# Optimization experiments

Measured on AMD Instinct MI355X. Metric: run time of the kernel, lower is better.

The kernel has to match this reference:

```python
import jax, jax.numpy as jnp
import numpy as np

MASK_THR = 0.005   # cfg.mask_thr
SIGMA = 2.0        # cfg.sigma (gaussian kernel)
N, G, H, W = 500, 128, 200, 304


def setup_inputs() -> dict:
    key = jax.random.key(0)
    k1, k2, k3, k4, k5, k6 = jax.random.split(key, 6)
    return {
        "cate_scores": jax.random.uniform(k1, (N,), jnp.float32),
        "seg_preds_x": jax.random.uniform(k2, (G, H, W), jnp.float32),
        "seg_preds_y": jax.random.uniform(k3, (G, H, W), jnp.float32),
        "cate_labels": jax.random.randint(k4, (N,), 0, 80),
        "x_inds": jax.random.randint(k5, (N,), 0, G),
        "y_inds": jax.random.randint(k6, (N,), 0, G),
    }


def reference(cate_scores, seg_preds_x, seg_preds_y, cate_labels, x_inds, y_inds):
    # --- SOLO decoupled mask decoding: irregular grid-index gather ---
    mask_x = seg_preds_x[x_inds]                 # [N,H,W]
    mask_y = seg_preds_y[y_inds]                 # [N,H,W]
    soft = mask_x * mask_y                       # seg_masks_soft
    hard = (soft > MASK_THR).astype(soft.dtype)  # seg_masks (binary)
    sum_masks = hard.sum((1, 2))                 # [N] mask areas
    # mask-quality rescoring
    seg_score = (soft * hard).sum((1, 2)) / jnp.maximum(sum_masks, 1.0)
    scores = cate_scores * seg_score

    # --- Matrix NMS (gaussian kernel) ---
    flat = hard.reshape(N, -1)                   # [N, H*W]
    inter = flat @ flat.T                        # [N,N] intersection areas
    union = sum_masks[:, None] + sum_masks[None, :] - inter
    iou = jnp.triu(inter / jnp.maximum(union, 1e-6), k=1)
    label_eq = jnp.triu((cate_labels[:, None] == cate_labels[None, :]).astype(soft.dtype), k=1)
    decay_iou = iou * label_eq                   # same-class IoU, upper tri
    comp_iou = decay_iou.max(0)                  # [N] max IoU with higher-scored same-class mask
    decay_matrix = jnp.exp(-SIGMA * decay_iou ** 2)
    comp_matrix = jnp.exp(-SIGMA * comp_iou ** 2)[:, None]  # expand(n,n).T in torch
    decay_coef = (decay_matrix / comp_matrix).min(0)         # [N]
    return scores * decay_coef
```

## Files before the change

kernel.cpp:

```cpp
#include <hip/hip_runtime.h>


#define N_DET 500
#define HW    (200 * 304)
#define NGROUP 238
#define NWORDS 952
#define NW2    476
#define MASK_THR 0.005f
#define SIGMA 2.0f

__global__ __launch_bounds__(512) void maskgen_kernel(
    const float* __restrict__ seg_x, const float* __restrict__ seg_y,
    const int* __restrict__ x_inds, const int* __restrict__ y_inds,
    unsigned long long* __restrict__ packed,
    float* __restrict__ part_sum,
    int*   __restrict__ part_cnt)
{
    const int b = blockIdx.x;
    const int n = b >> 1;
    const int s = b & 1;
    const float* __restrict__ rx = seg_x + (size_t)x_inds[n] * HW;
    const float* __restrict__ ry = seg_y + (size_t)y_inds[n] * HW;
    unsigned long long* __restrict__ pk = packed + (size_t)n * NWORDS;

    const int tid  = threadIdx.x;
    const int lane = tid & 63;
    const int wav  = tid >> 6;

    float ssum = 0.0f;
    int   cnt  = 0;
    const int gend = s * 119 + 119;
    for (int g = s * 119 + wav; g < gend; g += 8) {
        const int base = (g << 8) + (lane << 2);
        float4 x, y;
        if (base + 3 < HW) {
            x = *(const float4*)(rx + base);
            y = *(const float4*)(ry + base);
        } else {
            x = make_float4(0.f, 0.f, 0.f, 0.f);
            y = x;
        }
        const float p0 = x.x * y.x, p1 = x.y * y.y, p2 = x.z * y.z, p3 = x.w * y.w;
        const bool h0 = p0 > MASK_THR, h1 = p1 > MASK_THR,
                   h2 = p2 > MASK_THR, h3 = p3 > MASK_THR;
        const unsigned long long m0 = __ballot(h0), m1 = __ballot(h1),
                                 m2 = __ballot(h2), m3 = __ballot(h3);
        if (lane < 4) {
            const unsigned long long mv = (lane == 0) ? m0 : (lane == 1) ? m1
                                        : (lane == 2) ? m2 : m3;
            pk[(g << 2) + lane] = mv;
        }
        ssum += (h0 ? p0 : 0.f) + (h1 ? p1 : 0.f) + (h2 ? p2 : 0.f) + (h3 ? p3 : 0.f);
        cnt  += (int)h0 + (int)h1 + (int)h2 + (int)h3;
    }
    #pragma unroll
    for (int off = 32; off; off >>= 1) {
        ssum += __shfl_down(ssum, off);
        cnt  += __shfl_down(cnt,  off);
    }
    __shared__ float s_s[8];
    __shared__ int   s_c[8];
    if (lane == 0) { s_s[wav] = ssum; s_c[wav] = cnt; }
    __syncthreads();
    if (tid == 0) {
        float S = 0.f; int C = 0;
        #pragma unroll
        for (int q = 0; q < 8; ++q) { S += s_s[q]; C += s_c[q]; }
        part_sum[b] = S;
        part_cnt[b] = C;
    }
}

__global__ __launch_bounds__(512) void finalize_kernel(
    const float* __restrict__ part_sum, const int* __restrict__ part_cnt,
    const float* __restrict__ cate_scores,
    float* __restrict__ sum_masks, float* __restrict__ scores)
{
    const int n = threadIdx.x;
    if (n < N_DET) {
        const float S = part_sum[2 * n] + part_sum[2 * n + 1];
        const int   C = part_cnt[2 * n] + part_cnt[2 * n + 1];
        const float sm = (float)C;
        sum_masks[n] = sm;
        scores[n] = cate_scores[n] * (S / fmaxf(sm, 1.0f));
    }
}

__global__ __launch_bounds__(256) void pair_iou_kernel(
    const unsigned long long* __restrict__ packed,
    const float* __restrict__ sum_masks,
    const int* __restrict__ labels,
    float* __restrict__ d2col,
    float* __restrict__ comp2)
{
    const int j   = blockIdx.x;
    const int tid = threadIdx.x;
    const int lane = tid & 63, wav = tid >> 6;

    __shared__ int   s_lab[N_DET];
    __shared__ float s_sm[N_DET];
    __shared__ int   s_list[N_DET];
    __shared__ int   s_cnt;
    __shared__ float s_max[4];

    if (tid == 0) s_cnt = 0;
    for (int i = tid; i < N_DET; i += 256) {
        s_lab[i] = labels[i];
        s_sm[i]  = sum_masks[i];
        d2col[(size_t)j * N_DET + i] = 0.0f;
    }
    __syncthreads();

    const int   lj = s_lab[j];
    const float sj = s_sm[j];
    for (int i = tid; i < j; i += 256)
        if (s_lab[i] == lj) { const int p = atomicAdd(&s_cnt, 1); s_list[p] = i; }
    __syncthreads();
    const int cnt = s_cnt;

    const ulonglong2* __restrict__ pj2 = (const ulonglong2*)(packed + (size_t)j * NWORDS);
    ulonglong2 bj[8];
    #pragma unroll
    for (int t = 0; t < 8; ++t) {
        const int w = lane + (t << 6);
        if (w < NW2) bj[t] = pj2[w];
        else { bj[t].x = 0ull; bj[t].y = 0ull; }
    }

    float wmax = 0.0f;
    for (int p = wav; p < cnt; p += 4) {
        const int i = s_list[p];
        const ulonglong2* __restrict__ pi2 = (const ulonglong2*)(packed + (size_t)i * NWORDS);
        int part = 0;
        #pragma unroll
        for (int t = 0; t < 8; ++t) {
            const int w = lane + (t << 6);
            if (w < NW2) {
                const ulonglong2 a = pi2[w];
                part += __popcll(a.x & bj[t].x) + __popcll(a.y & bj[t].y);
            }
        }
        #pragma unroll
        for (int off = 32; off; off >>= 1) part += __shfl_down(part, off);
        if (lane == 0) {
            const float uni = s_sm[i] + sj - (float)part;
            const float iou = (float)part / fmaxf(uni, 1e-6f);
            d2col[(size_t)j * N_DET + i] = iou * iou;
            wmax = fmaxf(wmax, iou);
        }
    }
    if (lane == 0) s_max[wav] = wmax;
    __syncthreads();
    if (tid == 0) {
        const float c = fmaxf(fmaxf(s_max[0], s_max[1]), fmaxf(s_max[2], s_max[3]));
        comp2[j] = c * c;
    }
}

__global__ __launch_bounds__(64) void decay_kernel(
    const float* __restrict__ d2col,
    const float* __restrict__ comp2,
    const float* __restrict__ scores,
    float* __restrict__ out)
{
    const int j = blockIdx.x;
    const int lane = threadIdx.x;
    float m = 1e30f;
    for (int i = lane; i < N_DET; i += 64)
        m = fminf(m, comp2[i] - d2col[(size_t)j * N_DET + i]);
    #pragma unroll
    for (int off = 32; off; off >>= 1)
        m = fminf(m, __shfl_down(m, off));
    if (lane == 0) out[j] = scores[j] * expf(SIGMA * m);
}

extern "C" void kernel_launch(void* const* d_in, const int* in_sizes, int n_in,
                              void* d_out, int out_size, void* d_ws, size_t ws_size,
                              hipStream_t stream) {
    const float* cate_scores = (const float*)d_in[0];
    const float* seg_x       = (const float*)d_in[1];
    const float* seg_y       = (const float*)d_in[2];
    const int*   labels      = (const int*)d_in[3];
    const int*   x_inds      = (const int*)d_in[4];
    const int*   y_inds      = (const int*)d_in[5];
    float* out = (float*)d_out;

    char* ws = (char*)d_ws;
    unsigned long long* packed = (unsigned long long*)(ws + 0);
    float* d2col     = (float*)(ws + 3808000);
    float* part_sum  = (float*)(ws + 4808000);
    int*   part_cnt  = (int*)  (ws + 4812000);
    float* scores    = (float*)(ws + 4816000);
    float* comp2     = (float*)(ws + 4818000);
    float* sum_masks = (float*)(ws + 4820000);

    maskgen_kernel <<<N_DET * 2, 512, 0, stream>>>(seg_x, seg_y, x_inds, y_inds,
                                                   packed, part_sum, part_cnt);
    finalize_kernel<<<1, 512, 0, stream>>>(part_sum, part_cnt, cate_scores,
                                           sum_masks, scores);
    pair_iou_kernel<<<N_DET, 256, 0, stream>>>(packed, sum_masks, labels, d2col, comp2);
    decay_kernel   <<<N_DET, 64, 0, stream>>>(d2col, comp2, scores, out);
}
```

Baseline: 131.3 us.

## Tile mask generation over pixels to share grid rows across all detections

```diff
diff --git a/kernel.cpp b/kernel.cpp
--- a/kernel.cpp
+++ b/kernel.cpp
@@ -3,9 +3,11 @@
 
 #define N_DET 500
 #define HW    (200 * 304)
-#define NGROUP 238
-#define NWORDS 952
-#define NW2    476
+#define TILE  64
+#define NT    (HW / TILE)
+#define NWORDS NT
+#define NW2   (NWORDS / 2)
+#define LSTR  65
 #define MASK_THR 0.005f
 #define SIGMA 2.0f
 
@@ -16,70 +18,65 @@
     float* __restrict__ part_sum,
     int*   __restrict__ part_cnt)
 {
-    const int b = blockIdx.x;
-    const int n = b >> 1;
-    const int s = b & 1;
-    const float* __restrict__ rx = seg_x + (size_t)x_inds[n] * HW;
-    const float* __restrict__ ry = seg_y + (size_t)y_inds[n] * HW;
-    unsigned long long* __restrict__ pk = packed + (size_t)n * NWORDS;
-
-    const int tid  = threadIdx.x;
-    const int lane = tid & 63;
-    const int wav  = tid >> 6;
-
-    float ssum = 0.0f;
-    int   cnt  = 0;
-    const int gend = s * 119 + 119;
-    for (int g = s * 119 + wav; g < gend; g += 8) {
-        const int base = (g << 8) + (lane << 2);
-        float4 x, y;
-        if (base + 3 < HW) {
-            x = *(const float4*)(rx + base);
-            y = *(const float4*)(ry + base);
-        } else {
-            x = make_float4(0.f, 0.f, 0.f, 0.f);
-            y = x;
-        }
-        const float p0 = x.x * y.x, p1 = x.y * y.y, p2 = x.z * y.z, p3 = x.w * y.w;
-        const bool h0 = p0 > MASK_THR, h1 = p1 > MASK_THR,
-                   h2 = p2 > MASK_THR, h3 = p3 > MASK_THR;
-        const unsigned long long m0 = __ballot(h0), m1 = __ballot(h1),
-                                 m2 = __ballot(h2), m3 = __ballot(h3);
-        if (lane < 4) {
-            const unsigned long long mv = (lane == 0) ? m0 : (lane == 1) ? m1
-                                        : (lane == 2) ? m2 : m3;
-            pk[(g << 2) + lane] = mv;
-        }
-        ssum += (h0 ? p0 : 0.f) + (h1 ? p1 : 0.f) + (h2 ? p2 : 0.f) + (h3 ? p3 : 0.f);
-        cnt  += (int)h0 + (int)h1 + (int)h2 + (int)h3;
-    }
-    #pragma unroll
-    for (int off = 32; off; off >>= 1) {
-        ssum += __shfl_down(ssum, off);
-        cnt  += __shfl_down(cnt,  off);
-    }
-    __shared__ float s_s[8];
-    __shared__ int   s_c[8];
-    if (lane == 0) { s_s[wav] = ssum; s_c[wav] = cnt; }
-    __syncthreads();
-    if (tid == 0) {
-        float S = 0.f; int C = 0;
-        #pragma unroll
-        for (int q = 0; q < 8; ++q) { S += s_s[q]; C += s_c[q]; }
-        part_sum[b] = S;
-        part_cnt[b] = C;
-    }
-}
-
-__global__ __launch_bounds__(512) void finalize_kernel(
+    __shared__ float sx[128 * LSTR];
+    __shared__ float sy[128 * LSTR];
+    const int t   = blockIdx.x;
+    const int tid = threadIdx.x;
+    const int base_g = t * TILE;
+
+    for (int e = tid; e < 128 * 16; e += 512) {
+        const int r  = e >> 4;
+        const int c4 = (e & 15) << 2;
+        const float4 vx = *(const float4*)(seg_x + (size_t)r * HW + base_g + c4);
+        const float4 vy = *(const float4*)(seg_y + (size_t)r * HW + base_g + c4);
+        float* dx = sx + r * LSTR + c4;
+        float* dy = sy + r * LSTR + c4;
+        dx[0] = vx.x; dx[1] = vx.y; dx[2] = vx.z; dx[3] = vx.w;
+        dy[0] = vy.x; dy[1] = vy.y; dy[2] = vy.z; dy[3] = vy.w;
+    }
+    __syncthreads();
+
+    const int n = tid;
+    if (n < N_DET) {
+        const float* __restrict__ rx = sx + x_inds[n] * LSTR;
+        const float* __restrict__ ry = sy + y_inds[n] * LSTR;
+        float ssum = 0.0f;
+        int   cnt  = 0;
+        unsigned int lo = 0u, hi = 0u;
+        #pragma unroll
+        for (int p = 0; p < 32; ++p) {
+            const float v = rx[p] * ry[p];
+            if (v > MASK_THR) { ssum += v; ++cnt; lo |= (1u << p); }
+        }
+        #pragma unroll
+        for (int p = 0; p < 32; ++p) {
+            const float v = rx[32 + p] * ry[32 + p];
+            if (v > MASK_THR) { ssum += v; ++cnt; hi |= (1u << p); }
+        }
+        packed[(size_t)n * NWORDS + t] = ((unsigned long long)hi << 32) | lo;
+        part_sum[(size_t)t * N_DET + n] = ssum;
+        part_cnt[(size_t)t * N_DET + n] = cnt;
+    }
+}
+
+__global__ __launch_bounds__(64) void finalize_kernel(
     const float* __restrict__ part_sum, const int* __restrict__ part_cnt,
     const float* __restrict__ cate_scores,
     float* __restrict__ sum_masks, float* __restrict__ scores)
 {
-    const int n = threadIdx.x;
-    if (n < N_DET) {
-        const float S = part_sum[2 * n] + part_sum[2 * n + 1];
-        const int   C = part_cnt[2 * n] + part_cnt[2 * n + 1];
+    const int n    = blockIdx.x;
+    const int lane = threadIdx.x;
+    float S = 0.0f; int C = 0;
+    for (int t = lane; t < NT; t += 64) {
+        S += part_sum[(size_t)t * N_DET + n];
+        C += part_cnt[(size_t)t * N_DET + n];
+    }
+    #pragma unroll
+    for (int off = 32; off; off >>= 1) {
+        S += __shfl_down(S, off);
+        C += __shfl_down(C, off);
+    }
+    if (lane == 0) {
         const float sm = (float)C;
         sum_masks[n] = sm;
         scores[n] = cate_scores[n] * (S / fmaxf(sm, 1.0f));
@@ -187,17 +184,17 @@
 
     char* ws = (char*)d_ws;
     unsigned long long* packed = (unsigned long long*)(ws + 0);
-    float* d2col     = (float*)(ws + 3808000);
-    float* part_sum  = (float*)(ws + 4808000);
-    int*   part_cnt  = (int*)  (ws + 4812000);
-    float* scores    = (float*)(ws + 4816000);
-    float* comp2     = (float*)(ws + 4818000);
-    float* sum_masks = (float*)(ws + 4820000);
-
-    maskgen_kernel <<<N_DET * 2, 512, 0, stream>>>(seg_x, seg_y, x_inds, y_inds,
-                                                   packed, part_sum, part_cnt);
-    finalize_kernel<<<1, 512, 0, stream>>>(part_sum, part_cnt, cate_scores,
-                                           sum_masks, scores);
+    float* d2col     = (float*)(ws + 3800000);
+    float* part_sum  = (float*)(ws + 4800000);
+    int*   part_cnt  = (int*)  (ws + 6700000);
+    float* scores    = (float*)(ws + 8600000);
+    float* comp2     = (float*)(ws + 8602048);
+    float* sum_masks = (float*)(ws + 8604096);
+
+    maskgen_kernel <<<NT, 512, 0, stream>>>(seg_x, seg_y, x_inds, y_inds,
+                                            packed, part_sum, part_cnt);
+    finalize_kernel<<<N_DET, 64, 0, stream>>>(part_sum, part_cnt, cate_scores,
+                                              sum_masks, scores);
     pair_iou_kernel<<<N_DET, 256, 0, stream>>>(packed, sum_masks, labels, d2col, comp2);
     decay_kernel   <<<N_DET, 64, 0, stream>>>(d2col, comp2, scores, out);
 }
```

Result: slower. 135.1 us (+2.9%).
